# Optimization experiments

Measured on AMD Instinct MI355X. Metric: run time of the kernel, lower is better.

Reference implementation:

```python
import jax, jax.numpy as jnp
import numpy as np

N = 50000
E = 800000
NUM_GRAPHS = 64
D_IN = 261
D_SAGE = 64
D_LIN = 32
N_SAGE_REST = 6
N_LIN_REST = 3
EPS = 1e-5


def _layernorm(x, g, b):
    mu = jnp.mean(x, axis=-1, keepdims=True)
    var = jnp.mean((x - mu) ** 2, axis=-1, keepdims=True)
    return (x - mu) * jax.lax.rsqrt(var + EPS) * g + b


def _sage_block(x, Wl, bl, Wr, g, b, src, dst, inv_deg, residual):
    # mean aggregation of neighbor (source) features onto targets
    msum = jax.ops.segment_sum(x[src], dst, num_segments=N)  # [N, d]
    mean = msum * inv_deg  # [N, d]
    f = mean @ Wl + bl + x @ Wr  # lin_l(aggr) + lin_r(x); lin_r has no bias
    f = jax.nn.gelu(f, approximate=False)
    f = _layernorm(f, g, b)
    if residual:
        f = f + x
    return f


def _lin_block(x, W, b, g, beta, residual):
    f = jax.nn.gelu(x @ W + b, approximate=False)
    f = _layernorm(f, g, beta)
    if residual:
        f = f + x
    return f


def setup_inputs() -> dict:
    key = jax.random.key(0)
    ks = jax.random.split(key, 24)
    x = jax.random.normal(ks[0], (N, D_IN), dtype=jnp.float32)
    edge_index = jax.random.randint(ks[1], (2, E), 0, N, dtype=jnp.int64)
    batch = jnp.sort(jax.random.randint(ks[2], (N,), 0, NUM_GRAPHS, dtype=jnp.int64))

    def glorot(k, shape):
        fan_in = shape[0]
        return jax.random.normal(k, shape, dtype=jnp.float32) / np.sqrt(fan_in)

    inp = {
        "x": x, "edge_index": edge_index, "batch": batch,
        # first SAGE block (261 -> 64, no residual)
        "Wl0": glorot(ks[3], (D_IN, D_SAGE)), "bl0": jnp.zeros((D_SAGE,), jnp.float32),
        "Wr0": glorot(ks[4], (D_IN, D_SAGE)),
        "g0": jnp.ones((D_SAGE,), jnp.float32), "beta0": jnp.zeros((D_SAGE,), jnp.float32),
        # 6 residual SAGE blocks (64 -> 64), stacked
        "Wl": glorot(ks[5], (N_SAGE_REST, D_SAGE, D_SAGE)),
        "bl": jnp.zeros((N_SAGE_REST, D_SAGE), jnp.float32),
        "Wr": glorot(ks[6], (N_SAGE_REST, D_SAGE, D_SAGE)),
        "g": jnp.ones((N_SAGE_REST, D_SAGE), jnp.float32),
        "beta": jnp.zeros((N_SAGE_REST, D_SAGE), jnp.float32),
        # MLP: first LinearBlock 64 -> 32 (no residual)
        "M0": glorot(ks[7], (D_SAGE, D_LIN)), "mb0": jnp.zeros((D_LIN,), jnp.float32),
        "mg0": jnp.ones((D_LIN,), jnp.float32), "mbeta0": jnp.zeros((D_LIN,), jnp.float32),
        # 3 residual LinearBlocks 32 -> 32, stacked
        "M": glorot(ks[8], (N_LIN_REST, D_LIN, D_LIN)),
        "mb": jnp.zeros((N_LIN_REST, D_LIN), jnp.float32),
        "mg": jnp.ones((N_LIN_REST, D_LIN), jnp.float32),
        "mbeta": jnp.zeros((N_LIN_REST, D_LIN), jnp.float32),
        # final Linear 32 -> 1
        "Wf": glorot(ks[9], (D_LIN, 1)), "bf": jnp.zeros((1,), jnp.float32),
    }
    return inp


def reference(x, edge_index, batch, Wl0, bl0, Wr0, g0, beta0, Wl, bl, Wr, g, beta,
              M0, mb0, mg0, mbeta0, M, mb, mg, mbeta, Wf, bf):
    src, dst = edge_index[0], edge_index[1]
    deg = jax.ops.segment_sum(jnp.ones((E,), x.dtype), dst, num_segments=N)
    inv_deg = (1.0 / jnp.maximum(deg, 1.0))[:, None]  # [N,1]

    h = _sage_block(x, Wl0, bl0, Wr0, g0, beta0, src, dst, inv_deg, residual=False)
    for i in range(N_SAGE_REST):
        h = _sage_block(h, Wl[i], bl[i], Wr[i], g[i], beta[i], src, dst, inv_deg, residual=True)

    pooled = jax.ops.segment_sum(h, batch, num_segments=NUM_GRAPHS)  # [G, 64]

    m = _lin_block(pooled, M0, mb0, mg0, mbeta0, residual=False)
    for i in range(N_LIN_REST):
        m = _lin_block(m, M[i], mb[i], mg[i], mbeta[i], residual=True)
    return m @ Wf + bf  # [G, 1]
```

## Files before the change

### kernel.cpp

```cpp
#include <hip/hip_runtime.h>
#include <hip/hip_bf16.h>
#include <math.h>

#define N_NODES 50000
#define N_EDGES 800000
#define NUM_GRAPHS 64
#define NPAD 50048
#define KPAD0 288
#define PSPLIT 16
#define MAXDEG 64

#define G0_GRID    (NPAD / 32)
#define LAYER_GRID (NPAD / 32)
#define ZERO_GRID  ((N_NODES + 255) / 256)
#define PREPW_TOT  (128 * KPAD0 + 6 * 128 * 64)
#define PREPW_GRID ((PREPW_TOT + 255) / 256)
#define CONV_GRID  (NPAD * (KPAD0 / 8) / 256)

#define SLICES 8
#define NPS 6250
#define SCHUNK 2048
#define SCHUNKS ((N_EDGES + SCHUNK - 1) / SCHUNK)
#define SCAT_GRID (SCHUNKS * SLICES)

typedef __attribute__((ext_vector_type(8))) short short8;
typedef __attribute__((ext_vector_type(4))) float f32x4;

__device__ __forceinline__ float gelu_f(float v) {
    return 0.5f * v * (1.0f + erff(v * 0.70710678118654752440f));
}

__device__ __forceinline__ float half_sum32(float v) {
    v += __shfl_xor(v, 1); v += __shfl_xor(v, 2); v += __shfl_xor(v, 4);
    v += __shfl_xor(v, 8); v += __shfl_xor(v, 16);
    return v;
}

__device__ __forceinline__ float group_sum8(float v) {
    v += __shfl_xor(v, 1); v += __shfl_xor(v, 2); v += __shfl_xor(v, 4);
    return v;
}

__device__ __forceinline__ unsigned short f2bf(float f) {
    unsigned int u = __float_as_uint(f);
    unsigned int r = (u + 0x7fffu + ((u >> 16) & 1u)) >> 16;
    return (unsigned short)r;
}

__device__ __forceinline__ float bf_lo(unsigned int u) {
    return __uint_as_float(u << 16);
}
__device__ __forceinline__ float bf_hi(unsigned int u) {
    return __uint_as_float(u & 0xffff0000u);
}


__global__ void k_prep(int* __restrict__ deg,
                       const float* __restrict__ Wl0, const float* __restrict__ Wr0,
                       const float* __restrict__ Wl, const float* __restrict__ Wr,
                       unsigned short* __restrict__ Bt0, unsigned short* __restrict__ BtR,
                       const float* __restrict__ X, unsigned short* __restrict__ Xbf) {
    const int blk = blockIdx.x, tid = threadIdx.x;
    if (blk < ZERO_GRID) {
        int i = blk * 256 + tid;
        if (i < N_NODES) deg[i] = 0;
        return;
    }
    if (blk < ZERO_GRID + PREPW_GRID) {
        int idx = (blk - ZERO_GRID) * 256 + tid;
        const int n0 = 128 * KPAD0;
        if (idx < n0) {
            int j = idx / KPAD0, k = idx - j * KPAD0;
            float v = 0.0f;
            if (k < 261) v = (j < 64) ? Wl0[k * 64 + j] : Wr0[k * 64 + (j - 64)];
            Bt0[idx] = f2bf(v);
        } else if (idx < PREPW_TOT) {
            int r = idx - n0;
            int l = r >> 13;
            int rr = r & 8191;
            int j = rr >> 6, k = rr & 63;
            float v = (j < 64) ? Wl[l * 4096 + k * 64 + j] : Wr[l * 4096 + k * 64 + (j - 64)];
            BtR[r] = f2bf(v);
        }
        return;
    }
    int t = (blk - ZERO_GRID - PREPW_GRID) * 256 + tid;
    int node = t / (KPAD0 / 8);
    int k8 = (t - node * (KPAD0 / 8)) * 8;
    short8 v8;
    if (node < N_NODES) {
        #pragma unroll
        for (int j = 0; j < 8; ++j) {
            int k = k8 + j;
            float val = (k < 261) ? X[(size_t)node * 261 + k] : 0.0f;
            v8[j] = (short)f2bf(val);
        }
    } else {
        #pragma unroll
        for (int j = 0; j < 8; ++j) v8[j] = 0;
    }
    *(short8*)&Xbf[(size_t)node * KPAD0 + k8] = v8;
}


__global__ __launch_bounds__(256) void k_scat(
        const int* __restrict__ src, const int* __restrict__ dst,
        int* __restrict__ deg, unsigned short* __restrict__ col64) {
    const int s = blockIdx.x & (SLICES - 1);
    const int c = blockIdx.x >> 3;
    const int base = c * SCHUNK;
    const int lim = min(base + SCHUNK, N_EDGES);
    for (int i = base + (int)threadIdx.x; i < lim; i += 256) {
        int d = dst[i];
        if (d / NPS == s) {
            int sv = src[i];
            int pos = atomicAdd(&deg[d], 1);
            if (pos < MAXDEG) col64[(d << 6) + pos] = (unsigned short)sv;
        }
    }
}


__global__ __launch_bounds__(256) void k_gemm0(
        const unsigned short* __restrict__ Xbf, const unsigned short* __restrict__ Bt0,
        unsigned short* __restrict__ U, float* __restrict__ V) {
    __shared__ __align__(16) unsigned short sB[64 * 296];
    const int tid = threadIdx.x;
    const int lane = tid & 63, wid = tid >> 6;
    const int l16 = lane & 15, quad = lane >> 4;
    const int ch = blockIdx.x & 1;
    const int m0 = (blockIdx.x >> 1) * 64;
    #pragma unroll
    for (int k = 0; k < 9; ++k) {
        int g = k * 256 + tid;
        int row = g / 36;
        int part = (g - row * 36) * 8;
        *(short8*)&sB[row * 296 + part] =
            *(const short8*)&Bt0[(size_t)(ch * 64 + row) * KPAD0 + part];
    }
    f32x4 acc[4];
    #pragma unroll
    for (int j = 0; j < 4; ++j) { acc[j][0] = 0.f; acc[j][1] = 0.f; acc[j][2] = 0.f; acc[j][3] = 0.f; }
    const unsigned short* xr = Xbf + (size_t)(m0 + wid * 16 + l16) * KPAD0 + quad * 8;
    __syncthreads();
    for (int kc = 0; kc < KPAD0; kc += 32) {
        short8 af = *(const short8*)(xr + kc);
        #pragma unroll
        for (int j = 0; j < 4; ++j) {
            short8 bfv = *(const short8*)&sB[(j * 16 + l16) * 296 + kc + quad * 8];
            acc[j] = __builtin_amdgcn_mfma_f32_16x16x32_bf16(af, bfv, acc[j], 0, 0, 0);
        }
    }
    const int rbase = m0 + wid * 16 + quad * 4;
    if (ch == 0) {
        #pragma unroll
        for (int j = 0; j < 4; ++j)
            #pragma unroll
            for (int r = 0; r < 4; ++r)
                U[(size_t)(rbase + r) * 64 + j * 16 + l16] = f2bf(acc[j][r]);
    } else {
        #pragma unroll
        for (int j = 0; j < 4; ++j)
            #pragma unroll
            for (int r = 0; r < 4; ++r)
                V[(size_t)(rbase + r) * 64 + j * 16 + l16] = acc[j][r];
    }
}


__global__ __launch_bounds__(256) void k_layer(
        const unsigned short* __restrict__ U_in, const float* __restrict__ V_in,
        unsigned short* __restrict__ h,
        float* __restrict__ hf_out,
        const int* __restrict__ deg, const unsigned short* __restrict__ col64,
        const float* __restrict__ bias, const float* __restrict__ gam,
        const float* __restrict__ bet,
        const unsigned short* __restrict__ Bt_next,
        unsigned short* __restrict__ U_out, float* __restrict__ V_out,
        int residual, int have_gemm) {
    __shared__ __align__(16) unsigned short sA[2 * 32 * 32];
    __shared__ __align__(16) unsigned short sB[128 * 72];
    const int tid = threadIdx.x;
    const int lane = tid & 63, wid = tid >> 6;
    const int sub = lane >> 3, hl = lane & 7;
    const int base = lane & 56;
    const int m0 = blockIdx.x * 32;
    const uint4* __restrict__ Up = (const uint4*)U_in;

    if (have_gemm) {
        #pragma unroll
        for (int k = 0; k < 4; ++k) {
            int g = k * 256 + tid;
            int row = g >> 3, part = (g & 7) * 8;
            *(short8*)&sB[row * 72 + part] = *(const short8*)&Bt_next[(size_t)row * 64 + part];
        }
    }

    const int nl = wid * 8 + sub;
    const int node = m0 + nl;
    const bool valid = (node < N_NODES);
    const int nd = valid ? node : 0;
    const int dg = valid ? deg[nd] : 0;
    const int cnt = min(dg, MAXDEG);
    uint4 cv = make_uint4(0u, 0u, 0u, 0u);
    if (valid) cv = *(const uint4*)&col64[((size_t)nd << 6) + hl * 8];
    float s0 = 0.f, s1 = 0.f, s2 = 0.f, s3 = 0.f, s4 = 0.f, s5 = 0.f, s6 = 0.f, s7 = 0.f;
    for (int b = 0; b * 8 < cnt; b += 2) {
        #pragma unroll
        for (int hh = 0; hh < 2; ++hh) {
            const int sl = base + b + hh;
            unsigned int p0 = (unsigned int)__shfl((int)cv.x, sl);
            unsigned int p1 = (unsigned int)__shfl((int)cv.y, sl);
            unsigned int p2 = (unsigned int)__shfl((int)cv.z, sl);
            unsigned int p3 = (unsigned int)__shfl((int)cv.w, sl);
            const int eb = (b + hh) * 8;
            int c[8];
            c[0] = (int)(p0 & 0xffffu); c[1] = (int)(p0 >> 16);
            c[2] = (int)(p1 & 0xffffu); c[3] = (int)(p1 >> 16);
            c[4] = (int)(p2 & 0xffffu); c[5] = (int)(p2 >> 16);
            c[6] = (int)(p3 & 0xffffu); c[7] = (int)(p3 >> 16);
            #pragma unroll
            for (int i = 0; i < 8; ++i) {
                uint4 u = (eb + i < cnt) ? Up[(size_t)c[i] * 8 + hl] : make_uint4(0u, 0u, 0u, 0u);
                s0 += bf_lo(u.x); s1 += bf_hi(u.x);
                s2 += bf_lo(u.y); s3 += bf_hi(u.y);
                s4 += bf_lo(u.z); s5 += bf_hi(u.z);
                s6 += bf_lo(u.w); s7 += bf_hi(u.w);
            }
        }
    }
    const float id = 1.0f / fmaxf((float)dg, 1.0f);
    const float4 b0 = *(const float4*)&bias[8 * hl];
    const float4 b1 = *(const float4*)&bias[8 * hl + 4];
    float4 v0 = make_float4(0.f, 0.f, 0.f, 0.f), v1 = v0;
    if (valid) {
        v0 = *(const float4*)&V_in[(size_t)nd * 64 + 8 * hl];
        v1 = *(const float4*)&V_in[(size_t)nd * 64 + 8 * hl + 4];
    }
    float f0 = gelu_f(s0 * id + b0.x + v0.x);
    float f1 = gelu_f(s1 * id + b0.y + v0.y);
    float f2 = gelu_f(s2 * id + b0.z + v0.z);
    float f3 = gelu_f(s3 * id + b0.w + v0.w);
    float f4 = gelu_f(s4 * id + b1.x + v1.x);
    float f5 = gelu_f(s5 * id + b1.y + v1.y);
    float f6 = gelu_f(s6 * id + b1.z + v1.z);
    float f7 = gelu_f(s7 * id + b1.w + v1.w);
    float mu = group_sum8(((f0 + f1) + (f2 + f3)) + ((f4 + f5) + (f6 + f7))) * 0.015625f;
    float d0 = f0 - mu, d1 = f1 - mu, d2 = f2 - mu, d3 = f3 - mu;
    float d4 = f4 - mu, d5 = f5 - mu, d6 = f6 - mu, d7 = f7 - mu;
    float var = group_sum8(((d0 * d0 + d1 * d1) + (d2 * d2 + d3 * d3)) +
                           ((d4 * d4 + d5 * d5) + (d6 * d6 + d7 * d7))) * 0.015625f;
    float rs = rsqrtf(var + 1e-5f);
    const float4 g0v = *(const float4*)&gam[8 * hl];
    const float4 g1v = *(const float4*)&gam[8 * hl + 4];
    const float4 e0v = *(const float4*)&bet[8 * hl];
    const float4 e1v = *(const float4*)&bet[8 * hl + 4];
    f0 = d0 * rs * g0v.x + e0v.x;
    f1 = d1 * rs * g0v.y + e0v.y;
    f2 = d2 * rs * g0v.z + e0v.z;
    f3 = d3 * rs * g0v.w + e0v.w;
    f4 = d4 * rs * g1v.x + e1v.x;
    f5 = d5 * rs * g1v.y + e1v.y;
    f6 = d6 * rs * g1v.z + e1v.z;
    f7 = d7 * rs * g1v.w + e1v.w;
    if (residual && valid) {
        uint4 hu = ((const uint4*)h)[(size_t)nd * 8 + hl];
        f0 += bf_lo(hu.x); f1 += bf_hi(hu.x);
        f2 += bf_lo(hu.y); f3 += bf_hi(hu.y);
        f4 += bf_lo(hu.z); f5 += bf_hi(hu.z);
        f6 += bf_lo(hu.w); f7 += bf_hi(hu.w);
    }
    uint4 outw;
    outw.x = (unsigned int)f2bf(f0) | ((unsigned int)f2bf(f1) << 16);
    outw.y = (unsigned int)f2bf(f2) | ((unsigned int)f2bf(f3) << 16);
    outw.z = (unsigned int)f2bf(f4) | ((unsigned int)f2bf(f5) << 16);
    outw.w = (unsigned int)f2bf(f6) | ((unsigned int)f2bf(f7) << 16);
    if (valid) {
        ((uint4*)h)[(size_t)nd * 8 + hl] = outw;
        if (hf_out) {
            *(float4*)&hf_out[(size_t)nd * 64 + 8 * hl] = make_float4(f0, f1, f2, f3);
            *(float4*)&hf_out[(size_t)nd * 64 + 8 * hl + 4] = make_float4(f4, f5, f6, f7);
        }
    }
    *(uint4*)&sA[(((hl >> 2) * 32 + nl) << 5) + (hl & 3) * 8] = outw;

    if (!have_gemm) return;
    __syncthreads();

    const int l16 = lane & 15, quad = lane >> 4;
    const int wrow = wid & 1, colh = wid >> 1;
    f32x4 acc[4];
    #pragma unroll
    for (int j = 0; j < 4; ++j) { acc[j][0] = 0.f; acc[j][1] = 0.f; acc[j][2] = 0.f; acc[j][3] = 0.f; }
    #pragma unroll
    for (int kc = 0; kc < 64; kc += 32) {
        short8 af = *(const short8*)&sA[(((kc >> 5) * 32 + wrow * 16 + l16) << 5) + quad * 8];
        #pragma unroll
        for (int j = 0; j < 4; ++j) {
            short8 bfv = *(const short8*)&sB[(colh * 64 + j * 16 + l16) * 72 + kc + quad * 8];
            acc[j] = __builtin_amdgcn_mfma_f32_16x16x32_bf16(af, bfv, acc[j], 0, 0, 0);
        }
    }
    const int rbase = m0 + wrow * 16 + quad * 4;
    if (colh == 0) {
        #pragma unroll
        for (int j = 0; j < 4; ++j)
            #pragma unroll
            for (int r = 0; r < 4; ++r)
                U_out[(size_t)(rbase + r) * 64 + j * 16 + l16] = f2bf(acc[j][r]);
    } else {
        #pragma unroll
        for (int j = 0; j < 4; ++j)
            #pragma unroll
            for (int r = 0; r < 4; ++r)
                V_out[(size_t)(rbase + r) * 64 + j * 16 + l16] = acc[j][r];
    }
}


__global__ __launch_bounds__(256) void k_pool1(const float* __restrict__ h, const int* __restrict__ batch,
                                               float* __restrict__ partial, int n) {
    __shared__ float sred[4][64];
    const int g = blockIdx.x / PSPLIT;
    const int s = blockIdx.x - g * PSPLIT;
    const int lane = threadIdx.x & 63, wid = threadIdx.x >> 6;
    int lo = 0, hi = n;
    while (lo < hi) { int mid = (lo + hi) >> 1; if (batch[mid] < g) lo = mid + 1; else hi = mid; }
    const int start = lo;
    lo = 0; hi = n;
    while (lo < hi) { int mid = (lo + hi) >> 1; if (batch[mid] < g + 1) lo = mid + 1; else hi = mid; }
    const int end = lo;
    const int len = end - start;
    const int chunk = (len + PSPLIT - 1) / PSPLIT;
    const int a = start + s * chunk;
    const int b = min(a + chunk, end);
    float sum = 0.0f;
    for (int node = a + wid; node < b; node += 4) sum += h[(size_t)node * 64 + lane];
    sred[wid][lane] = sum;
    __syncthreads();
    if (wid == 0)
        partial[(size_t)blockIdx.x * 64 + lane] = sred[0][lane] + sred[1][lane] + sred[2][lane] + sred[3][lane];
}


__global__ __launch_bounds__(1024) void k_head(const float* __restrict__ partial,
                                               const float* __restrict__ M0, const float* __restrict__ mb0,
                                               const float* __restrict__ mg0, const float* __restrict__ mbeta0,
                                               const float* __restrict__ M, const float* __restrict__ mb,
                                               const float* __restrict__ mg, const float* __restrict__ mbeta,
                                               const float* __restrict__ Wf, const float* __restrict__ bf,
                                               float* __restrict__ out) {
    __shared__ float sP[64 * 64];
    __shared__ float sA[64 * 33];
    __shared__ float sB[64 * 33];
    const int tx = threadIdx.x, ty = threadIdx.y;
    const int tid = ty * 32 + tx;
    for (int i = tid; i < 64 * 64; i += 1024) {
        int g = i >> 6, f = i & 63;
        float s = 0.0f;
        #pragma unroll
        for (int s2 = 0; s2 < PSPLIT; ++s2) s += partial[(size_t)(g * PSPLIT + s2) * 64 + f];
        sP[i] = s;
    }
    __syncthreads();
    #pragma unroll
    for (int rr = 0; rr < 2; ++rr) {
        int r = ty + rr * 32;
        float a = mb0[tx];
        for (int k = 0; k < 64; ++k) a += sP[r * 64 + k] * M0[k * 32 + tx];
        a = gelu_f(a);
        float mu = half_sum32(a) * (1.0f / 32.0f);
        float d = a - mu;
        float var = half_sum32(d * d) * (1.0f / 32.0f);
        a = d * rsqrtf(var + 1e-5f) * mg0[tx] + mbeta0[tx];
        sA[r * 33 + tx] = a;
    }
    __syncthreads();
    float* cur = sA;
    float* nxt = sB;
    for (int L = 0; L < 3; ++L) {
        const float* Mi = M + L * 32 * 32;
        const float* mbi = mb + L * 32;
        const float* mgi = mg + L * 32;
        const float* mbetai = mbeta + L * 32;
        #pragma unroll
        for (int rr = 0; rr < 2; ++rr) {
            int r = ty + rr * 32;
            float a = mbi[tx];
            for (int k = 0; k < 32; ++k) a += cur[r * 33 + k] * Mi[k * 32 + tx];
            a = gelu_f(a);
            float mu = half_sum32(a) * (1.0f / 32.0f);
            float d = a - mu;
            float var = half_sum32(d * d) * (1.0f / 32.0f);
            a = d * rsqrtf(var + 1e-5f) * mgi[tx] + mbetai[tx] + cur[r * 33 + tx];
            nxt[r * 33 + tx] = a;
        }
        __syncthreads();
        float* t = cur; cur = nxt; nxt = t;
    }
    #pragma unroll
    for (int rr = 0; rr < 2; ++rr) {
        int r = ty + rr * 32;
        float p = cur[r * 33 + tx] * Wf[tx];
        p = half_sum32(p);
        if (tx == 0) out[r] = p + bf[0];
    }
}


extern "C" void kernel_launch(void* const* d_in, const int* in_sizes, int n_in,
                              void* d_out, int out_size, void* d_ws, size_t ws_size,
                              hipStream_t stream) {
    const int N = N_NODES;
    const int E = N_EDGES;

    const float* x    = (const float*)d_in[0];
    const int* eidx   = (const int*)d_in[1];
    const int* batch  = (const int*)d_in[2];
    const float* Wl0  = (const float*)d_in[3];
    const float* bl0  = (const float*)d_in[4];
    const float* Wr0  = (const float*)d_in[5];
    const float* g0   = (const float*)d_in[6];
    const float* bet0 = (const float*)d_in[7];
    const float* Wl   = (const float*)d_in[8];
    const float* bl   = (const float*)d_in[9];
    const float* Wr   = (const float*)d_in[10];
    const float* gR   = (const float*)d_in[11];
    const float* betR = (const float*)d_in[12];
    const float* M0   = (const float*)d_in[13];
    const float* mb0  = (const float*)d_in[14];
    const float* mg0  = (const float*)d_in[15];
    const float* mbe0 = (const float*)d_in[16];
    const float* M    = (const float*)d_in[17];
    const float* mb   = (const float*)d_in[18];
    const float* mg   = (const float*)d_in[19];
    const float* mbe  = (const float*)d_in[20];
    const float* Wf   = (const float*)d_in[21];
    const float* bf   = (const float*)d_in[22];

    const int* src = eidx;
    const int* dst = eidx + E;

    char* p = (char*)d_ws;
    auto alloc = [&](size_t bytes) -> void* {
        void* q = (void*)p;
        p += (bytes + 255) & ~(size_t)255;
        return q;
    };
    int*   deg    = (int*)alloc((size_t)N * 4);
    unsigned short* col64 = (unsigned short*)alloc((size_t)N * MAXDEG * 2);
    unsigned short* Bt0 = (unsigned short*)alloc((size_t)128 * KPAD0 * 2);
    unsigned short* BtR = (unsigned short*)alloc((size_t)6 * 128 * 64 * 2);
    unsigned short* Xbf = (unsigned short*)alloc((size_t)NPAD * KPAD0 * 2);
    unsigned short* Ua  = (unsigned short*)alloc((size_t)NPAD * 64 * 2);
    unsigned short* Ub  = (unsigned short*)alloc((size_t)NPAD * 64 * 2);
    float* Va   = (float*)alloc((size_t)NPAD * 64 * 4);
    float* Vb   = (float*)alloc((size_t)NPAD * 64 * 4);
    unsigned short* hbuf = (unsigned short*)alloc((size_t)NPAD * 64 * 2);
    float* partial = (float*)alloc((size_t)NUM_GRAPHS * PSPLIT * 64 * 4);

    k_prep<<<ZERO_GRID + PREPW_GRID + CONV_GRID, 256, 0, stream>>>(
        deg, Wl0, Wr0, Wl, Wr, Bt0, BtR, x, Xbf);

    k_scat<<<SCAT_GRID, 256, 0, stream>>>(src, dst, deg, col64);

    k_gemm0<<<G0_GRID, 256, 0, stream>>>(Xbf, Bt0, Ua, Va);

    unsigned short* Uin = Ua;  float* Vin = Va;
    unsigned short* Uout = Ub; float* Vout = Vb;
    for (int i = 0; i < 7; ++i) {
        const float* bias = (i == 0) ? bl0  : bl  + (size_t)(i - 1) * 64;
        const float* gam  = (i == 0) ? g0   : gR  + (size_t)(i - 1) * 64;
        const float* bet  = (i == 0) ? bet0 : betR + (size_t)(i - 1) * 64;
        const int have_gemm = (i < 6);
        float* hf = (i == 6) ? Vout : nullptr;
        k_layer<<<LAYER_GRID, 256, 0, stream>>>(
            Uin, Vin, hbuf, hf, deg, col64, bias, gam, bet,
            have_gemm ? (BtR + (size_t)i * 128 * 64) : BtR,
            Uout, Vout, (i > 0) ? 1 : 0, have_gemm);
        unsigned short* tu = Uin; Uin = Uout; Uout = tu;
        float* tv = Vin; Vin = Vout; Vout = tv;
    }
    float* hf_final = Vin;

    k_pool1<<<NUM_GRAPHS * PSPLIT, 256, 0, stream>>>(hf_final, batch, partial, N);
    k_head<<<1, dim3(32, 32), 0, stream>>>(partial, M0, mb0, mg0, mbe0, M, mb, mg, mbe, Wf, bf, (float*)d_out);
}
```

Before: 394.7 us.

## Fuse edge scatter into prep kernel and fold graph pooling into last layer

Merges the edge scatter kernel with the weight/feature conversion kernel into one front launch, replacing the degree-zeroing blocks with a memset that also clears the pooling buffer. The final SAGE layer now reduces its outputs per graph with wave shuffles and atomically adds them into the per-graph partial buffer, removing the fp32 feature write and the separate pooling kernel. This saves two kernel launches and one full pass over the node features. In exchange it adds float atomics with nondeterministic summation order, and a shared front kernel whose scatter blocks may contend with the conversion blocks.

```diff
diff --git a/kernel.cpp b/kernel.cpp
--- a/kernel.cpp
+++ b/kernel.cpp
@@ -12,7 +12,6 @@
 
 #define G0_GRID    (NPAD / 32)
 #define LAYER_GRID (NPAD / 32)
-#define ZERO_GRID  ((N_NODES + 255) / 256)
 #define PREPW_TOT  (128 * KPAD0 + 6 * 128 * 64)
 #define PREPW_GRID ((PREPW_TOT + 255) / 256)
 #define CONV_GRID  (NPAD * (KPAD0 / 8) / 256)
@@ -22,6 +21,7 @@
 #define SCHUNK 2048
 #define SCHUNKS ((N_EDGES + SCHUNK - 1) / SCHUNK)
 #define SCAT_GRID (SCHUNKS * SLICES)
+#define FRONT_GRID (SCAT_GRID + CONV_GRID + PREPW_GRID)
 
 typedef __attribute__((ext_vector_type(8))) short short8;
 typedef __attribute__((ext_vector_type(4))) float f32x4;
@@ -55,68 +55,63 @@
 }
 
 
-__global__ void k_prep(int* __restrict__ deg,
-                       const float* __restrict__ Wl0, const float* __restrict__ Wr0,
-                       const float* __restrict__ Wl, const float* __restrict__ Wr,
-                       unsigned short* __restrict__ Bt0, unsigned short* __restrict__ BtR,
-                       const float* __restrict__ X, unsigned short* __restrict__ Xbf) {
-    const int blk = blockIdx.x, tid = threadIdx.x;
-    if (blk < ZERO_GRID) {
-        int i = blk * 256 + tid;
-        if (i < N_NODES) deg[i] = 0;
+__global__ __launch_bounds__(256) void k_front(
+        const int* __restrict__ src, const int* __restrict__ dst,
+        int* __restrict__ deg, unsigned short* __restrict__ col64,
+        const float* __restrict__ X, unsigned short* __restrict__ Xbf,
+        const float* __restrict__ Wl0, const float* __restrict__ Wr0,
+        const float* __restrict__ Wl, const float* __restrict__ Wr,
+        unsigned short* __restrict__ Bt0, unsigned short* __restrict__ BtR) {
+    const int blk = blockIdx.x;
+    const int tid = threadIdx.x;
+    if (blk < SCAT_GRID) {
+        const int s = blk & (SLICES - 1);
+        const int c = blk >> 3;
+        const int base = c * SCHUNK;
+        const int lim = min(base + SCHUNK, N_EDGES);
+        for (int i = base + tid; i < lim; i += 256) {
+            int d = dst[i];
+            if (d / NPS == s) {
+                int sv = src[i];
+                int pos = atomicAdd(&deg[d], 1);
+                if (pos < MAXDEG) col64[(d << 6) + pos] = (unsigned short)sv;
+            }
+        }
         return;
     }
-    if (blk < ZERO_GRID + PREPW_GRID) {
-        int idx = (blk - ZERO_GRID) * 256 + tid;
-        const int n0 = 128 * KPAD0;
-        if (idx < n0) {
-            int j = idx / KPAD0, k = idx - j * KPAD0;
-            float v = 0.0f;
-            if (k < 261) v = (j < 64) ? Wl0[k * 64 + j] : Wr0[k * 64 + (j - 64)];
-            Bt0[idx] = f2bf(v);
-        } else if (idx < PREPW_TOT) {
-            int r = idx - n0;
-            int l = r >> 13;
-            int rr = r & 8191;
-            int j = rr >> 6, k = rr & 63;
-            float v = (j < 64) ? Wl[l * 4096 + k * 64 + j] : Wr[l * 4096 + k * 64 + (j - 64)];
-            BtR[r] = f2bf(v);
-        }
+    if (blk < SCAT_GRID + CONV_GRID) {
+        int t = (blk - SCAT_GRID) * 256 + tid;
+        int node = t / (KPAD0 / 8);
+        int k8 = (t - node * (KPAD0 / 8)) * 8;
+        short8 v8;
+        if (node < N_NODES) {
+            #pragma unroll
+            for (int j = 0; j < 8; ++j) {
+                int k = k8 + j;
+                float val = (k < 261) ? X[(size_t)node * 261 + k] : 0.0f;
+                v8[j] = (short)f2bf(val);
+            }
+        } else {
+            #pragma unroll
+            for (int j = 0; j < 8; ++j) v8[j] = 0;
+        }
+        *(short8*)&Xbf[(size_t)node * KPAD0 + k8] = v8;
         return;
     }
-    int t = (blk - ZERO_GRID - PREPW_GRID) * 256 + tid;
-    int node = t / (KPAD0 / 8);
-    int k8 = (t - node * (KPAD0 / 8)) * 8;
-    short8 v8;
-    if (node < N_NODES) {
-        #pragma unroll
-        for (int j = 0; j < 8; ++j) {
-            int k = k8 + j;
-            float val = (k < 261) ? X[(size_t)node * 261 + k] : 0.0f;
-            v8[j] = (short)f2bf(val);
-        }
-    } else {
-        #pragma unroll
-        for (int j = 0; j < 8; ++j) v8[j] = 0;
-    }
-    *(short8*)&Xbf[(size_t)node * KPAD0 + k8] = v8;
-}
-
-
-__global__ __launch_bounds__(256) void k_scat(
-        const int* __restrict__ src, const int* __restrict__ dst,
-        int* __restrict__ deg, unsigned short* __restrict__ col64) {
-    const int s = blockIdx.x & (SLICES - 1);
-    const int c = blockIdx.x >> 3;
-    const int base = c * SCHUNK;
-    const int lim = min(base + SCHUNK, N_EDGES);
-    for (int i = base + (int)threadIdx.x; i < lim; i += 256) {
-        int d = dst[i];
-        if (d / NPS == s) {
-            int sv = src[i];
-            int pos = atomicAdd(&deg[d], 1);
-            if (pos < MAXDEG) col64[(d << 6) + pos] = (unsigned short)sv;
-        }
+    int idx = (blk - SCAT_GRID - CONV_GRID) * 256 + tid;
+    const int n0 = 128 * KPAD0;
+    if (idx < n0) {
+        int j = idx / KPAD0, k = idx - j * KPAD0;
+        float v = 0.0f;
+        if (k < 261) v = (j < 64) ? Wl0[k * 64 + j] : Wr0[k * 64 + (j - 64)];
+        Bt0[idx] = f2bf(v);
+    } else if (idx < PREPW_TOT) {
+        int r = idx - n0;
+        int l = r >> 13;
+        int rr = r & 8191;
+        int j = rr >> 6, k = rr & 63;
+        float v = (j < 64) ? Wl[l * 4096 + k * 64 + j] : Wr[l * 4096 + k * 64 + (j - 64)];
+        BtR[r] = f2bf(v);
     }
 }
 
@@ -171,12 +166,12 @@
 __global__ __launch_bounds__(256) void k_layer(
         const unsigned short* __restrict__ U_in, const float* __restrict__ V_in,
         unsigned short* __restrict__ h,
-        float* __restrict__ hf_out,
         const int* __restrict__ deg, const unsigned short* __restrict__ col64,
         const float* __restrict__ bias, const float* __restrict__ gam,
         const float* __restrict__ bet,
         const unsigned short* __restrict__ Bt_next,
         unsigned short* __restrict__ U_out, float* __restrict__ V_out,
+        const int* __restrict__ batch, float* __restrict__ pool_part,
         int residual, int have_gemm) {
     __shared__ __align__(16) unsigned short sA[2 * 32 * 32];
     __shared__ __align__(16) unsigned short sB[128 * 72];
@@ -270,18 +265,49 @@
         f4 += bf_lo(hu.z); f5 += bf_hi(hu.z);
         f6 += bf_lo(hu.w); f7 += bf_hi(hu.w);
     }
+
+    if (pool_part) {
+        const int myg = valid ? batch[nd] : -1;
+        const int i_lo = (m0 < N_NODES) ? m0 : (N_NODES - 1);
+        const int i_hi = (m0 + 31 < N_NODES) ? (m0 + 31) : (N_NODES - 1);
+        const int g_lo = batch[i_lo];
+        const int g_hi = batch[i_hi];
+        const int split = blockIdx.x & (PSPLIT - 1);
+        for (int g = g_lo; g <= g_hi; ++g) {
+            const bool mine = (myg == g);
+            float p0 = mine ? f0 : 0.f, p1 = mine ? f1 : 0.f;
+            float p2 = mine ? f2 : 0.f, p3 = mine ? f3 : 0.f;
+            float p4 = mine ? f4 : 0.f, p5 = mine ? f5 : 0.f;
+            float p6 = mine ? f6 : 0.f, p7 = mine ? f7 : 0.f;
+            p0 += __shfl_xor(p0, 8);  p1 += __shfl_xor(p1, 8);
+            p2 += __shfl_xor(p2, 8);  p3 += __shfl_xor(p3, 8);
+            p4 += __shfl_xor(p4, 8);  p5 += __shfl_xor(p5, 8);
+            p6 += __shfl_xor(p6, 8);  p7 += __shfl_xor(p7, 8);
+            p0 += __shfl_xor(p0, 16); p1 += __shfl_xor(p1, 16);
+            p2 += __shfl_xor(p2, 16); p3 += __shfl_xor(p3, 16);
+            p4 += __shfl_xor(p4, 16); p5 += __shfl_xor(p5, 16);
+            p6 += __shfl_xor(p6, 16); p7 += __shfl_xor(p7, 16);
+            p0 += __shfl_xor(p0, 32); p1 += __shfl_xor(p1, 32);
+            p2 += __shfl_xor(p2, 32); p3 += __shfl_xor(p3, 32);
+            p4 += __shfl_xor(p4, 32); p5 += __shfl_xor(p5, 32);
+            p6 += __shfl_xor(p6, 32); p7 += __shfl_xor(p7, 32);
+            if (sub == 0) {
+                float* dp = &pool_part[((size_t)g * PSPLIT + split) * 64 + 8 * hl];
+                atomicAdd(dp + 0, p0); atomicAdd(dp + 1, p1);
+                atomicAdd(dp + 2, p2); atomicAdd(dp + 3, p3);
+                atomicAdd(dp + 4, p4); atomicAdd(dp + 5, p5);
+                atomicAdd(dp + 6, p6); atomicAdd(dp + 7, p7);
+            }
+        }
+        return;
+    }
+
     uint4 outw;
     outw.x = (unsigned int)f2bf(f0) | ((unsigned int)f2bf(f1) << 16);
     outw.y = (unsigned int)f2bf(f2) | ((unsigned int)f2bf(f3) << 16);
     outw.z = (unsigned int)f2bf(f4) | ((unsigned int)f2bf(f5) << 16);
     outw.w = (unsigned int)f2bf(f6) | ((unsigned int)f2bf(f7) << 16);
-    if (valid) {
-        ((uint4*)h)[(size_t)nd * 8 + hl] = outw;
-        if (hf_out) {
-            *(float4*)&hf_out[(size_t)nd * 64 + 8 * hl] = make_float4(f0, f1, f2, f3);
-            *(float4*)&hf_out[(size_t)nd * 64 + 8 * hl + 4] = make_float4(f4, f5, f6, f7);
-        }
-    }
+    if (valid) ((uint4*)h)[(size_t)nd * 8 + hl] = outw;
     *(uint4*)&sA[(((hl >> 2) * 32 + nl) << 5) + (hl & 3) * 8] = outw;
 
     if (!have_gemm) return;
@@ -315,31 +341,6 @@
             for (int r = 0; r < 4; ++r)
                 V_out[(size_t)(rbase + r) * 64 + j * 16 + l16] = acc[j][r];
     }
-}
-
-
-__global__ __launch_bounds__(256) void k_pool1(const float* __restrict__ h, const int* __restrict__ batch,
-                                               float* __restrict__ partial, int n) {
-    __shared__ float sred[4][64];
-    const int g = blockIdx.x / PSPLIT;
-    const int s = blockIdx.x - g * PSPLIT;
-    const int lane = threadIdx.x & 63, wid = threadIdx.x >> 6;
-    int lo = 0, hi = n;
-    while (lo < hi) { int mid = (lo + hi) >> 1; if (batch[mid] < g) lo = mid + 1; else hi = mid; }
-    const int start = lo;
-    lo = 0; hi = n;
-    while (lo < hi) { int mid = (lo + hi) >> 1; if (batch[mid] < g + 1) lo = mid + 1; else hi = mid; }
-    const int end = lo;
-    const int len = end - start;
-    const int chunk = (len + PSPLIT - 1) / PSPLIT;
-    const int a = start + s * chunk;
-    const int b = min(a + chunk, end);
-    float sum = 0.0f;
-    for (int node = a + wid; node < b; node += 4) sum += h[(size_t)node * 64 + lane];
-    sred[wid][lane] = sum;
-    __syncthreads();
-    if (wid == 0)
-        partial[(size_t)blockIdx.x * 64 + lane] = sred[0][lane] + sred[1][lane] + sred[2][lane] + sred[3][lane];
 }
 
 
@@ -447,7 +448,8 @@
         p += (bytes + 255) & ~(size_t)255;
         return q;
     };
-    int*   deg    = (int*)alloc((size_t)N * 4);
+    int*   deg     = (int*)alloc((size_t)N * 4);
+    float* partial = (float*)alloc((size_t)NUM_GRAPHS * PSPLIT * 64 * 4);
     unsigned short* col64 = (unsigned short*)alloc((size_t)N * MAXDEG * 2);
     unsigned short* Bt0 = (unsigned short*)alloc((size_t)128 * KPAD0 * 2);
     unsigned short* BtR = (unsigned short*)alloc((size_t)6 * 128 * 64 * 2);
@@ -457,12 +459,12 @@
     float* Va   = (float*)alloc((size_t)NPAD * 64 * 4);
     float* Vb   = (float*)alloc((size_t)NPAD * 64 * 4);
     unsigned short* hbuf = (unsigned short*)alloc((size_t)NPAD * 64 * 2);
-    float* partial = (float*)alloc((size_t)NUM_GRAPHS * PSPLIT * 64 * 4);
-
-    k_prep<<<ZERO_GRID + PREPW_GRID + CONV_GRID, 256, 0, stream>>>(
-        deg, Wl0, Wr0, Wl, Wr, Bt0, BtR, x, Xbf);
-
-    k_scat<<<SCAT_GRID, 256, 0, stream>>>(src, dst, deg, col64);
+
+    size_t zspan = (size_t)((char*)col64 - (char*)deg);
+    hipMemsetAsync(deg, 0, zspan, stream);
+
+    k_front<<<FRONT_GRID, 256, 0, stream>>>(
+        src, dst, deg, col64, x, Xbf, Wl0, Wr0, Wl, Wr, Bt0, BtR);
 
     k_gemm0<<<G0_GRID, 256, 0, stream>>>(Xbf, Bt0, Ua, Va);
 
@@ -473,16 +475,14 @@
         const float* gam  = (i == 0) ? g0   : gR  + (size_t)(i - 1) * 64;
         const float* bet  = (i == 0) ? bet0 : betR + (size_t)(i - 1) * 64;
         const int have_gemm = (i < 6);
-        float* hf = (i == 6) ? Vout : nullptr;
+        float* pool_part = (i == 6) ? partial : nullptr;
         k_layer<<<LAYER_GRID, 256, 0, stream>>>(
-            Uin, Vin, hbuf, hf, deg, col64, bias, gam, bet,
+            Uin, Vin, hbuf, deg, col64, bias, gam, bet,
             have_gemm ? (BtR + (size_t)i * 128 * 64) : BtR,
-            Uout, Vout, (i > 0) ? 1 : 0, have_gemm);
+            Uout, Vout, batch, pool_part, (i > 0) ? 1 : 0, have_gemm);
         unsigned short* tu = Uin; Uin = Uout; Uout = tu;
         float* tv = Vin; Vin = Vout; Vout = tv;
     }
-    float* hf_final = Vin;
-
-    k_pool1<<<NUM_GRAPHS * PSPLIT, 256, 0, stream>>>(hf_final, batch, partial, N);
+
     k_head<<<1, dim3(32, 32), 0, stream>>>(partial, M0, mb0, mg0, mbe0, M, mb, mg, mbe, Wf, bf, (float*)d_out);
 }
```

Measured after the change: 381.9 us. 1.03x faster.
